# Optimization experiments

Hardware: AMD Instinct MI355X
Metric: run time of the kernel (lower is better)

## Reference

```python
import jax, jax.numpy as jnp
import numpy as np


@jax.custom_vjp
def spike(mem, v_th):
    # Heaviside forward, triangular surrogate backward (gamma=1.0)
    return (mem >= v_th).astype(mem.dtype)


def _spike_fwd(mem, v_th):
    return spike(mem, v_th), (mem, v_th)


def _spike_bwd(res, g):
    mem, v_th = res
    surr = jnp.clip(1.0 - jnp.abs(mem - v_th), 0.0)  # gamma = 1
    return (g * surr, jnp.zeros_like(v_th))  # torch returns None for threshold grad


spike.defvjp(_spike_fwd, _spike_bwd)


def setup_inputs() -> dict:
    key = jax.random.key(0)
    ks = jax.random.split(key, 6)
    T, B, C, H, W = 8, 16, 256, 32, 32
    NH, HID = 4, 64
    x = jax.random.normal(ks[0], (T, B, C, H, W), dtype=jnp.float32)
    decay_param = jnp.float32(np.log(0.85 / 0.15))  # logit(0.85)
    v_th = jnp.float32(0.5)
    W1 = jax.random.normal(ks[1], (NH, HID, T), dtype=jnp.float32) * 0.1
    b1 = jax.random.normal(ks[2], (NH, HID), dtype=jnp.float32) * 0.01
    W2 = jax.random.normal(ks[3], (NH, T, HID), dtype=jnp.float32) * 0.1
    b2 = jax.random.normal(ks[4], (NH, T), dtype=jnp.float32) * 0.01
    att_w = jnp.ones((NH,), dtype=jnp.float32) / NH
    return {"x": x, "decay_param": decay_param, "v_th": v_th,
            "W1": W1, "b1": b1, "W2": W2, "b2": b2, "att_w": att_w}


def reference(x, decay_param, v_th, W1, b1, W2, b2, att_w):
    T, B, C, H, W = x.shape
    d = jax.nn.sigmoid(decay_param)

    def step(carry, inp):
        mem, spk = carry  # detached states, as in the torch module
        m = d * (mem - v_th * spk) + inp
        denom = jnp.mean(jnp.abs(m), axis=(1, 2, 3), keepdims=True) + 1e-6
        m = m / denom
        s = spike(m, v_th)
        carry = (jax.lax.stop_gradient(m), jax.lax.stop_gradient(s))
        return carry, s

    init = (jnp.zeros_like(x[0]), jnp.zeros_like(x[0]))
    _, spikes = jax.lax.scan(step, init, x)          # [T,B,C,H,W]

    feats = spikes.reshape(T, B, C * H * W)          # [T,B,F]
    summary = feats.mean(axis=2).T                   # [B,T]
    # multi-head MLP attention over time
    h = jax.nn.relu(jnp.einsum('bt,nht->bnh', summary, W1) + b1[None])  # [B,NH,HID]
    maps = jnp.einsum('bnh,nth->bnt', h, W2) + b2[None]                  # [B,NH,T]
    weighted = jnp.sum(maps * att_w[None, :, None], axis=1)              # [B,T]
    aw = jax.nn.softmax(weighted, axis=-1).T[:, :, None]                 # [T,B,1]
    out = jnp.sum(feats * aw, axis=0)                                    # [B,F]
    return out
```

## Files before the change

kernel.cpp:

```cpp
#include <hip/hip_runtime.h>

#define NT    8
#define NB    16
#define FS    262144
#define TPB   256
#define BPB   64
#define GRID  (NB*BPB)
#define CHK   4
#define ELB   (TPB*CHK*4)
#define SPIN_CAP (1L<<26)

#define WS_SMALL 66624
#define WS_FAST  99392

__global__ __launch_bounds__(TPB, 4)
void bispike_kernel(const float* __restrict__ x,
                    const float* __restrict__ decay_p,
                    const float* __restrict__ vth_p,
                    const float* __restrict__ W1,
                    const float* __restrict__ b1,
                    const float* __restrict__ W2,
                    const float* __restrict__ b2,
                    const float* __restrict__ att_w,
                    float* __restrict__ out,
                    double* __restrict__ bsum,
                    int* __restrict__ scnt,
                    int* __restrict__ ccnt,
                    int* __restrict__ cnt,
                    int fastcnt)
{
    const int tid  = threadIdx.x;
    const int lane = tid & 63;
    const int wid  = tid >> 6;
    const int b    = blockIdx.x / BPB;
    const int bg   = blockIdx.x % BPB;

    const double dec  = 1.0 / (1.0 + exp(-(double)decay_p[0]));
    const double vth  = (double)vth_p[0];
    const double csub = dec * vth;

    __shared__ double wv[NT][4];
    __shared__ double dn[NT];
    if (tid < NT * 4) ((double*)wv)[tid] = 0.0;
    if (tid < NT)     dn[tid] = 0.0;
    __syncthreads();

    double   u[CHK * 4];
    float4   xv[CHK];
    unsigned sm[NT];

    {
        const float* p = x + (size_t)b * FS + (size_t)bg * ELB + tid * 4;
        #pragma unroll
        for (int k = 0; k < CHK; ++k) xv[k] = *(const float4*)(p + k * (TPB * 4));
    }
    double lsum = 0.0;
    #pragma unroll
    for (int k = 0; k < CHK; ++k) {
        u[k*4+0] = (double)xv[k].x; u[k*4+1] = (double)xv[k].y;
        u[k*4+2] = (double)xv[k].z; u[k*4+3] = (double)xv[k].w;
        lsum += fabs(u[k*4+0]) + fabs(u[k*4+1]) + fabs(u[k*4+2]) + fabs(u[k*4+3]);
    }

    #pragma unroll 1
    for (int t = 0; t < NT; ++t) {
        if (t < NT - 1) {
            const float* p = x + ((size_t)(t + 1) * NB + b) * FS
                               + (size_t)bg * ELB + tid * 4;
            #pragma unroll
            for (int k = 0; k < CHK; ++k) xv[k] = *(const float4*)(p + k * (TPB * 4));
        }

        #pragma unroll
        for (int off = 32; off > 0; off >>= 1)
            lsum += __shfl_down(lsum, off, 64);
        if (lane == 0)
            __hip_atomic_store(&wv[t][wid], -lsum, __ATOMIC_RELAXED,
                               __HIP_MEMORY_SCOPE_WORKGROUP);

        if (wid == 0) {
            double w; long it = 0;
            for (;;) {
                w = __hip_atomic_load(&wv[t][lane & 3], __ATOMIC_RELAXED,
                                      __HIP_MEMORY_SCOPE_WORKGROUP);
                if (__all(__double_as_longlong(w) != 0)) break;
                if (++it > SPIN_CAP) break;
                __builtin_amdgcn_s_sleep(1);
            }
            w = -w;
            w += __shfl_down(w, 2, 64);
            w += __shfl_down(w, 1, 64);
            const double blk = __shfl(w, 0, 64);

            double* slot = bsum + (size_t)(t * NB + b) * BPB;
            if (lane == 0)
                __hip_atomic_store(slot + bg, -blk, __ATOMIC_RELAXED,
                                   __HIP_MEMORY_SCOPE_AGENT);

            double v = 0.0; it = 0;
            for (;;) {
                if (lane != bg)
                    v = __hip_atomic_load(slot + lane, __ATOMIC_RELAXED,
                                          __HIP_MEMORY_SCOPE_AGENT);
                if (__all(lane == bg || __double_as_longlong(v) != 0)) break;
                if (++it > SPIN_CAP) break;
                __builtin_amdgcn_s_sleep(1);
            }
            double tot = (lane == bg) ? blk : -v;
            #pragma unroll
            for (int off = 32; off > 0; off >>= 1)
                tot += __shfl_down(tot, off, 64);
            if (lane == 0)
                __hip_atomic_store(&dn[t], tot / (double)FS + 1e-6,
                                   __ATOMIC_RELAXED, __HIP_MEMORY_SCOPE_WORKGROUP);
        }

        double denom; long it2 = 0;
        for (;;) {
            denom = __hip_atomic_load(&dn[t], __ATOMIC_RELAXED,
                                      __HIP_MEMORY_SCOPE_WORKGROUP);
            if (__double_as_longlong(denom) != 0) break;
            if (++it2 > SPIN_CAP) break;
            __builtin_amdgcn_s_sleep(1);
        }

        const double thr = vth * denom;
        const double a   = dec * (1.0 / denom);
        unsigned smt = 0;
        if (t < NT - 1) {
            double nl = 0.0;
            #pragma unroll
            for (int k = 0; k < CHK; ++k) {
                const double xn0 = (double)xv[k].x, xn1 = (double)xv[k].y,
                             xn2 = (double)xv[k].z, xn3 = (double)xv[k].w;
                double un;
                bool s0 = (u[k*4+0] >= thr); if (s0) smt |= 1u << (k*4+0);
                un = fma(a, u[k*4+0], xn0); if (s0) un -= csub;
                u[k*4+0] = un; nl += fabs(un);
                bool s1 = (u[k*4+1] >= thr); if (s1) smt |= 1u << (k*4+1);
                un = fma(a, u[k*4+1], xn1); if (s1) un -= csub;
                u[k*4+1] = un; nl += fabs(un);
                bool s2 = (u[k*4+2] >= thr); if (s2) smt |= 1u << (k*4+2);
                un = fma(a, u[k*4+2], xn2); if (s2) un -= csub;
                u[k*4+2] = un; nl += fabs(un);
                bool s3 = (u[k*4+3] >= thr); if (s3) smt |= 1u << (k*4+3);
                un = fma(a, u[k*4+3], xn3); if (s3) un -= csub;
                u[k*4+3] = un; nl += fabs(un);
            }
            lsum = nl;
        } else {
            #pragma unroll
            for (int j = 0; j < CHK * 4; ++j)
                if (u[j] >= thr) smt |= 1u << j;
        }
        sm[t] = smt;
    }

    __shared__ int ired[NT][4];
    #pragma unroll
    for (int t = 0; t < NT; ++t) {
        int c = __popc(sm[t]);
        #pragma unroll
        for (int off = 32; off > 0; off >>= 1)
            c += __shfl_down(c, off, 64);
        if (lane == 0) ired[t][wid] = c;
    }
    __syncthreads();

    __shared__ double summ_s[NT];
    __shared__ int totc_s[NT];

    if (fastcnt) {
        if (tid < 64) {
            int* cb = cnt + b * (NT * BPB);
            if (tid < NT) {
                int tot = (ired[tid][0] + ired[tid][1])
                        + (ired[tid][2] + ired[tid][3]);
                __hip_atomic_store(cb + tid * BPB + bg, tot + 1,
                                   __ATOMIC_RELAXED, __HIP_MEMORY_SCOPE_AGENT);
            }
            int vt[NT]; long it = 0;
            for (;;) {
                bool ok = true;
                #pragma unroll
                for (int t = 0; t < NT; ++t) {
                    vt[t] = __hip_atomic_load(cb + t * BPB + tid,
                                              __ATOMIC_RELAXED,
                                              __HIP_MEMORY_SCOPE_AGENT);
                    ok = ok && (vt[t] > 0);
                }
                if (__all(ok)) break;
                if (++it > SPIN_CAP) break;
                __builtin_amdgcn_s_sleep(1);
            }
            #pragma unroll
            for (int t = 0; t < NT; ++t) {
                int s = vt[t] - 1;
                #pragma unroll
                for (int off = 32; off > 0; off >>= 1)
                    s += __shfl_down(s, off, 64);
                if (tid == 0) totc_s[t] = s;
            }
        }
        __syncthreads();
        if (tid < NT)
            summ_s[tid] = (double)totc_s[tid] / (double)FS;
    } else {
        if (tid < NT) {
            int tot = (ired[tid][0] + ired[tid][1]) + (ired[tid][2] + ired[tid][3]);
            __hip_atomic_fetch_add(&scnt[tid * NB + b], tot,
                                   __ATOMIC_RELEASE, __HIP_MEMORY_SCOPE_AGENT);
        }
        __syncthreads();
        if (tid == 0) {
            __hip_atomic_fetch_add(&ccnt[b], 1,
                                   __ATOMIC_RELEASE, __HIP_MEMORY_SCOPE_AGENT);
            long it = 0;
            while (__hip_atomic_load(&ccnt[b], __ATOMIC_ACQUIRE,
                                     __HIP_MEMORY_SCOPE_AGENT) < BPB
                   && it++ < SPIN_CAP)
                __builtin_amdgcn_s_sleep(4);
        }
        __syncthreads();
        if (tid < NT) {
            int c = __hip_atomic_load(&scnt[tid * NB + b],
                                      __ATOMIC_ACQUIRE, __HIP_MEMORY_SCOPE_AGENT);
            summ_s[tid] = (double)c / (double)FS;
        }
    }
    __syncthreads();

    __shared__ double h_s[4 * 64];
    __shared__ double wmat_s[NT];
    {
        int nh = tid >> 6, hd = tid & 63;
        double acc = 0.0;
        #pragma unroll
        for (int t = 0; t < NT; ++t)
            acc += summ_s[t] * (double)W1[nh * 512 + hd * 8 + t];
        acc += (double)b1[nh * 64 + hd];
        h_s[tid] = fmax(acc, 0.0);
    }
    __syncthreads();
    if (tid < NT) {
        double w = 0.0;
        for (int nh = 0; nh < 4; ++nh) {
            double macc = 0.0;
            for (int hd = 0; hd < 64; ++hd)
                macc += h_s[nh * 64 + hd] * (double)W2[nh * 512 + tid * 64 + hd];
            macc += (double)b2[nh * 8 + tid];
            w += macc * (double)att_w[nh];
        }
        wmat_s[tid] = w;
    }
    __syncthreads();

    double awr[NT];
    {
        double mx = wmat_s[0];
        #pragma unroll
        for (int t = 1; t < NT; ++t) mx = fmax(mx, wmat_s[t]);
        double ss = 0.0;
        #pragma unroll
        for (int t = 0; t < NT; ++t) { awr[t] = exp(wmat_s[t] - mx); ss += awr[t]; }
        #pragma unroll
        for (int t = 0; t < NT; ++t) awr[t] = awr[t] / ss;
    }

    float* po = out + (size_t)b * FS + (size_t)bg * ELB + tid * 4;
    #pragma unroll
    for (int k = 0; k < CHK; ++k) {
        double o[4] = {0.0, 0.0, 0.0, 0.0};
        #pragma unroll
        for (int t = 0; t < NT; ++t) {
            const unsigned smt = sm[t];
            o[0] += ((smt >> (k * 4 + 0)) & 1) ? awr[t] : 0.0;
            o[1] += ((smt >> (k * 4 + 1)) & 1) ? awr[t] : 0.0;
            o[2] += ((smt >> (k * 4 + 2)) & 1) ? awr[t] : 0.0;
            o[3] += ((smt >> (k * 4 + 3)) & 1) ? awr[t] : 0.0;
        }
        *(float4*)(po + k * (TPB * 4)) =
            make_float4((float)o[0], (float)o[1], (float)o[2], (float)o[3]);
    }
}

__global__ void diag_kernel(float* out, int code) {
    out[0] = 100000.0f + (float)code;
}

extern "C" void kernel_launch(void* const* d_in, const int* in_sizes, int n_in,
                              void* d_out, int out_size, void* d_ws, size_t ws_size,
                              hipStream_t stream) {
    const float* x     = (const float*)d_in[0];
    const float* decay = (const float*)d_in[1];
    const float* vth   = (const float*)d_in[2];
    const float* W1    = (const float*)d_in[3];
    const float* b1    = (const float*)d_in[4];
    const float* W2    = (const float*)d_in[5];
    const float* b2    = (const float*)d_in[6];
    const float* att   = (const float*)d_in[7];
    float* out = (float*)d_out;

    if (ws_size < WS_SMALL) {
        diag_kernel<<<1, 1, 0, stream>>>(out, 999);
        return;
    }
    const int fastcnt = (ws_size >= (size_t)WS_FAST) ? 1 : 0;

    double* bsum = (double*)d_ws;
    int*    scnt = (int*)((char*)d_ws + 65536);
    int*    ccnt = (int*)((char*)d_ws + 66048);
    int*    cnt  = (int*)((char*)d_ws + 66624);

    hipMemsetAsync(d_ws, 0, fastcnt ? WS_FAST : WS_SMALL, stream);

    hipGetLastError();
    bispike_kernel<<<dim3(GRID), dim3(TPB), 0, stream>>>(
        x, decay, vth, W1, b1, W2, b2, att, out, bsum, scnt, ccnt, cnt, fastcnt);
    hipError_t err = hipGetLastError();
    if (err != hipSuccess) {
        diag_kernel<<<1, 1, 0, stream>>>(out, (int)err);
    }
}
```

Measured before the change: 249.5 us.

## Halve blocks per batch, double per-thread chunk, simplify intra-block reduction sync

Cuts blocks per batch from 64 to 32 and doubles the elements each thread processes, so each cross-block barrier per timestep waits on fewer participants and the global grid is smaller. Block indices are interleaved across batches. The shared-memory atomic spin for the intra-block sum is replaced by plain __syncthreads-based reductions, and the absolute-value accumulations are split into four partial sums to shorten dependency chains. The cost is more registers per thread (launch bounds lowered to 2 blocks per SIMD occupancy hint) and less memory-level parallelism per step.

```diff
diff --git a/kernel.cpp b/kernel.cpp
--- a/kernel.cpp
+++ b/kernel.cpp
@@ -4,16 +4,16 @@
 #define NB    16
 #define FS    262144
 #define TPB   256
-#define BPB   64
+#define BPB   32
 #define GRID  (NB*BPB)
-#define CHK   4
+#define CHK   8
 #define ELB   (TPB*CHK*4)
 #define SPIN_CAP (1L<<26)
 
-#define WS_SMALL 66624
-#define WS_FAST  99392
-
-__global__ __launch_bounds__(TPB, 4)
+#define WS_SMALL 33344
+#define WS_FAST  49728
+
+__global__ __launch_bounds__(TPB, 2)
 void bispike_kernel(const float* __restrict__ x,
                     const float* __restrict__ decay_p,
                     const float* __restrict__ vth_p,
@@ -32,19 +32,13 @@
     const int tid  = threadIdx.x;
     const int lane = tid & 63;
     const int wid  = tid >> 6;
-    const int b    = blockIdx.x / BPB;
-    const int bg   = blockIdx.x % BPB;
+    const int b    = blockIdx.x % NB;
+    const int bg   = blockIdx.x / NB;
 
     const double dec  = 1.0 / (1.0 + exp(-(double)decay_p[0]));
     const double vth  = (double)vth_p[0];
     const double csub = dec * vth;
 
-    __shared__ double wv[NT][4];
-    __shared__ double dn[NT];
-    if (tid < NT * 4) ((double*)wv)[tid] = 0.0;
-    if (tid < NT)     dn[tid] = 0.0;
-    __syncthreads();
-
     double   u[CHK * 4];
     float4   xv[CHK];
     unsigned sm[NT];
@@ -54,13 +48,21 @@
         #pragma unroll
         for (int k = 0; k < CHK; ++k) xv[k] = *(const float4*)(p + k * (TPB * 4));
     }
-    double lsum = 0.0;
-    #pragma unroll
-    for (int k = 0; k < CHK; ++k) {
-        u[k*4+0] = (double)xv[k].x; u[k*4+1] = (double)xv[k].y;
-        u[k*4+2] = (double)xv[k].z; u[k*4+3] = (double)xv[k].w;
-        lsum += fabs(u[k*4+0]) + fabs(u[k*4+1]) + fabs(u[k*4+2]) + fabs(u[k*4+3]);
-    }
+    double lsum;
+    {
+        double n0 = 0.0, n1 = 0.0, n2 = 0.0, n3 = 0.0;
+        #pragma unroll
+        for (int k = 0; k < CHK; ++k) {
+            u[k*4+0] = (double)xv[k].x; n0 += fabs(u[k*4+0]);
+            u[k*4+1] = (double)xv[k].y; n1 += fabs(u[k*4+1]);
+            u[k*4+2] = (double)xv[k].z; n2 += fabs(u[k*4+2]);
+            u[k*4+3] = (double)xv[k].w; n3 += fabs(u[k*4+3]);
+        }
+        lsum = (n0 + n1) + (n2 + n3);
+    }
+
+    __shared__ double dred[4];
+    __shared__ double denom_s;
 
     #pragma unroll 1
     for (int t = 0; t < NT; ++t) {
@@ -71,64 +73,46 @@
             for (int k = 0; k < CHK; ++k) xv[k] = *(const float4*)(p + k * (TPB * 4));
         }
 
+        double ls = lsum;
         #pragma unroll
         for (int off = 32; off > 0; off >>= 1)
-            lsum += __shfl_down(lsum, off, 64);
-        if (lane == 0)
-            __hip_atomic_store(&wv[t][wid], -lsum, __ATOMIC_RELAXED,
-                               __HIP_MEMORY_SCOPE_WORKGROUP);
-
-        if (wid == 0) {
-            double w; long it = 0;
+            ls += __shfl_down(ls, off, 64);
+        if (lane == 0) dred[wid] = ls;
+        __syncthreads();
+
+        if (tid < 64) {
+            double bs = (dred[0] + dred[1]) + (dred[2] + dred[3]);
+            double* slot = bsum + (size_t)(t * NB + b) * BPB;
+            if (tid == 0)
+                __hip_atomic_store(slot + bg, -bs, __ATOMIC_RELAXED,
+                                   __HIP_MEMORY_SCOPE_AGENT);
+
+            const int  sl  = lane & 31;
+            const bool act = (lane < 32) && (sl != bg);
+            double v = 0.0; long it = 0;
             for (;;) {
-                w = __hip_atomic_load(&wv[t][lane & 3], __ATOMIC_RELAXED,
-                                      __HIP_MEMORY_SCOPE_WORKGROUP);
-                if (__all(__double_as_longlong(w) != 0)) break;
+                if (act)
+                    v = __hip_atomic_load(slot + sl, __ATOMIC_RELAXED,
+                                          __HIP_MEMORY_SCOPE_AGENT);
+                if (__all(!act || __double_as_longlong(v) != 0)) break;
                 if (++it > SPIN_CAP) break;
                 __builtin_amdgcn_s_sleep(1);
             }
-            w = -w;
-            w += __shfl_down(w, 2, 64);
-            w += __shfl_down(w, 1, 64);
-            const double blk = __shfl(w, 0, 64);
-
-            double* slot = bsum + (size_t)(t * NB + b) * BPB;
-            if (lane == 0)
-                __hip_atomic_store(slot + bg, -blk, __ATOMIC_RELAXED,
-                                   __HIP_MEMORY_SCOPE_AGENT);
-
-            double v = 0.0; it = 0;
-            for (;;) {
-                if (lane != bg)
-                    v = __hip_atomic_load(slot + lane, __ATOMIC_RELAXED,
-                                          __HIP_MEMORY_SCOPE_AGENT);
-                if (__all(lane == bg || __double_as_longlong(v) != 0)) break;
-                if (++it > SPIN_CAP) break;
-                __builtin_amdgcn_s_sleep(1);
-            }
-            double tot = (lane == bg) ? blk : -v;
+            double tot = (lane >= 32) ? 0.0 : ((sl == bg) ? bs : -v);
             #pragma unroll
             for (int off = 32; off > 0; off >>= 1)
                 tot += __shfl_down(tot, off, 64);
-            if (lane == 0)
-                __hip_atomic_store(&dn[t], tot / (double)FS + 1e-6,
-                                   __ATOMIC_RELAXED, __HIP_MEMORY_SCOPE_WORKGROUP);
-        }
-
-        double denom; long it2 = 0;
-        for (;;) {
-            denom = __hip_atomic_load(&dn[t], __ATOMIC_RELAXED,
-                                      __HIP_MEMORY_SCOPE_WORKGROUP);
-            if (__double_as_longlong(denom) != 0) break;
-            if (++it2 > SPIN_CAP) break;
-            __builtin_amdgcn_s_sleep(1);
-        }
+            if (tid == 0)
+                denom_s = tot / (double)FS + 1e-6;
+        }
+        __syncthreads();
+        const double denom = denom_s;
 
         const double thr = vth * denom;
         const double a   = dec * (1.0 / denom);
         unsigned smt = 0;
         if (t < NT - 1) {
-            double nl = 0.0;
+            double n0 = 0.0, n1 = 0.0, n2 = 0.0, n3 = 0.0;
             #pragma unroll
             for (int k = 0; k < CHK; ++k) {
                 const double xn0 = (double)xv[k].x, xn1 = (double)xv[k].y,
@@ -136,18 +120,18 @@
                 double un;
                 bool s0 = (u[k*4+0] >= thr); if (s0) smt |= 1u << (k*4+0);
                 un = fma(a, u[k*4+0], xn0); if (s0) un -= csub;
-                u[k*4+0] = un; nl += fabs(un);
+                u[k*4+0] = un; n0 += fabs(un);
                 bool s1 = (u[k*4+1] >= thr); if (s1) smt |= 1u << (k*4+1);
                 un = fma(a, u[k*4+1], xn1); if (s1) un -= csub;
-                u[k*4+1] = un; nl += fabs(un);
+                u[k*4+1] = un; n1 += fabs(un);
                 bool s2 = (u[k*4+2] >= thr); if (s2) smt |= 1u << (k*4+2);
                 un = fma(a, u[k*4+2], xn2); if (s2) un -= csub;
-                u[k*4+2] = un; nl += fabs(un);
+                u[k*4+2] = un; n2 += fabs(un);
                 bool s3 = (u[k*4+3] >= thr); if (s3) smt |= 1u << (k*4+3);
                 un = fma(a, u[k*4+3], xn3); if (s3) un -= csub;
-                u[k*4+3] = un; nl += fabs(un);
-            }
-            lsum = nl;
+                u[k*4+3] = un; n3 += fabs(un);
+            }
+            lsum = (n0 + n1) + (n2 + n3);
         } else {
             #pragma unroll
             for (int j = 0; j < CHK * 4; ++j)
@@ -179,15 +163,19 @@
                 __hip_atomic_store(cb + tid * BPB + bg, tot + 1,
                                    __ATOMIC_RELAXED, __HIP_MEMORY_SCOPE_AGENT);
             }
+            const int  sl  = lane & 31;
+            const bool act = (lane < 32) && (sl != bg);
             int vt[NT]; long it = 0;
             for (;;) {
                 bool ok = true;
                 #pragma unroll
                 for (int t = 0; t < NT; ++t) {
-                    vt[t] = __hip_atomic_load(cb + t * BPB + tid,
-                                              __ATOMIC_RELAXED,
-                                              __HIP_MEMORY_SCOPE_AGENT);
-                    ok = ok && (vt[t] > 0);
+                    if (act) {
+                        vt[t] = __hip_atomic_load(cb + t * BPB + sl,
+                                                  __ATOMIC_RELAXED,
+                                                  __HIP_MEMORY_SCOPE_AGENT);
+                        ok = ok && (vt[t] > 0);
+                    }
                 }
                 if (__all(ok)) break;
                 if (++it > SPIN_CAP) break;
@@ -195,7 +183,11 @@
             }
             #pragma unroll
             for (int t = 0; t < NT; ++t) {
-                int s = vt[t] - 1;
+                int s;
+                if (lane >= 32)      s = 0;
+                else if (sl == bg)   s = (ired[t][0] + ired[t][1])
+                                       + (ired[t][2] + ired[t][3]);
+                else                 s = vt[t] - 1;
                 #pragma unroll
                 for (int off = 32; off > 0; off >>= 1)
                     s += __shfl_down(s, off, 64);
@@ -308,9 +300,9 @@
     const int fastcnt = (ws_size >= (size_t)WS_FAST) ? 1 : 0;
 
     double* bsum = (double*)d_ws;
-    int*    scnt = (int*)((char*)d_ws + 65536);
-    int*    ccnt = (int*)((char*)d_ws + 66048);
-    int*    cnt  = (int*)((char*)d_ws + 66624);
+    int*    scnt = (int*)((char*)d_ws + 32768);
+    int*    ccnt = (int*)((char*)d_ws + 33280);
+    int*    cnt  = (int*)((char*)d_ws + 33344);
 
     hipMemsetAsync(d_ws, 0, fastcnt ? WS_FAST : WS_SMALL, stream);
 
```

Result: faster. 234.8 us (-5.9%).
